# Performance work log

Measured on AMD Instinct MI355X. Metric: run time of the kernel, lower is better.

## Reference

```python
import jax, jax.numpy as jnp
import numpy as np

B, N, D = 2, 2048, 1024
H = 16
HD = D // H  # 64
NEG = -1e30


def setup_inputs() -> dict:
    key = jax.random.key(0)
    ks = jax.random.split(key, 6)
    s = 0.02
    return {
        "x": jax.random.normal(ks[0], (B, N, D), dtype=jnp.float32),
        "Wq": jax.random.normal(ks[1], (D, D), dtype=jnp.float32) * s,
        "Wk": jax.random.normal(ks[2], (D, D), dtype=jnp.float32) * s,
        "Wv": jax.random.normal(ks[3], (D, D), dtype=jnp.float32) * s,
        "Wo": jax.random.normal(ks[4], (D, D), dtype=jnp.float32) * s,
        "Wf": jax.random.normal(ks[5], (D, H), dtype=jnp.float32) * s,
    }


def reference(x, Wq, Wk, Wv, Wo, Wf):
    b, n, d = x.shape
    h, hd = H, HD
    scale = hd ** -0.5
    # projections (Linear without bias; weights stored as [in, out])
    q = (x @ Wq).reshape(b, n, h, hd).transpose(0, 2, 1, 3)  # b h n hd
    k = (x @ Wk).reshape(b, n, h, hd).transpose(0, 2, 1, 3)
    v = (x @ Wv).reshape(b, n, h, hd).transpose(0, 2, 1, 3)
    # per-head log forget gate, cumulative sum over positions
    log_f = jax.nn.log_sigmoid(x @ Wf).transpose(0, 2, 1)  # b h n
    c = jnp.cumsum(log_f, axis=-1)  # b h n
    # scores with additive decay bias: bias[i,j] = c[i] - c[j] (j <= i)
    scores = jnp.einsum('bhid,bhjd->bhij', q, k) * scale
    scores = scores + c[..., :, None] - c[..., None, :]
    causal = jnp.tril(jnp.ones((n, n), dtype=bool))
    scores = jnp.where(causal, scores, NEG)
    attn = jax.nn.softmax(scores, axis=-1)
    out = jnp.einsum('bhij,bhjd->bhid', attn, v)  # b h n hd
    out = out.transpose(0, 2, 1, 3).reshape(b, n, d)
    return out @ Wo
```

## Files before the change

### kernel.cpp

```cpp
#include <hip/hip_runtime.h>
#include <hip/hip_bf16.h>
#include <stdint.h>

#define NN 2048
#define DD 1024
#define HH 16
#define HDD 64
#define QBLK 64
#define KVBLK 64

typedef unsigned short u16;
typedef __attribute__((ext_vector_type(8))) __bf16 bf16x8_t;
typedef __attribute__((ext_vector_type(4))) float f32x4_t;

static __device__ __forceinline__ u16 f2bf(float f) {
  union { float f; uint32_t u; } v; v.f = f;
  uint32_t r = v.u + 0x7FFFu + ((v.u >> 16) & 1u);
  return (u16)(r >> 16);
}

static __device__ __forceinline__ uint32_t packbf2(float a, float b) {
  __hip_bfloat162 h2 = __float22bfloat162_rn(make_float2(a, b));
  union { __hip_bfloat162 hh; uint32_t u; } cvt; cvt.hh = h2;
  return cvt.u;
}

static __device__ __forceinline__ void async_copy16(const void* g, void* l) {
  __builtin_amdgcn_global_load_lds((const __attribute__((address_space(1))) void*)g,
                                   (__attribute__((address_space(3))) void*)l, 16, 0, 0);
}

__global__ void prep_kernel(const float* __restrict__ x, const float* __restrict__ Wf,
                            float* __restrict__ lf, u16* __restrict__ xb,
                            const float* __restrict__ W0, const float* __restrict__ W1,
                            const float* __restrict__ W2, const float* __restrict__ W3,
                            u16* __restrict__ Wt) {
  __shared__ float xs[DD];
  __shared__ float part[16][17];
  __shared__ float tile[64][65];
  int t = threadIdx.x;
  if (blockIdx.x < 4096) {
    int row = blockIdx.x;
    float4 v = *(const float4*)&x[(size_t)row * DD + t * 4];
    *(float4*)&xs[t * 4] = v;
    ushort4 o;
    o.x = f2bf(v.x); o.y = f2bf(v.y); o.z = f2bf(v.z); o.w = f2bf(v.w);
    *(ushort4*)&xb[(size_t)row * DD + t * 4] = o;
    __syncthreads();
    int h = t & 15, chunk = t >> 4;
    float s = 0.f;
#pragma unroll 8
    for (int e = 0; e < 64; e++)
      s += xs[chunk * 64 + e] * Wf[(chunk * 64 + e) * HH + h];
    part[chunk][h] = s;
    __syncthreads();
    if (t < 16) {
      float z = 0.f;
#pragma unroll
      for (int i = 0; i < 16; i++) z += part[i][t];
      float ls = fminf(z, 0.f) - log1pf(__expf(-fabsf(z)));
      int b = row >> 11, n = row & (NN - 1);
      lf[(b * HH + t) * NN + n] = ls;
    }
  } else {
    int bid = blockIdx.x - 4096;
    int wq = bid >> 8;
    const float* W = wq == 0 ? W0 : wq == 1 ? W1 : wq == 2 ? W2 : W3;
    u16* out = Wt + (size_t)wq * DD * DD;
    int bx = bid & 15;
    int by = (bid >> 4) & 15;
    int c = t & 63, r4 = t >> 6;
#pragma unroll
    for (int i = 0; i < 16; i++) {
      int row = i * 4 + r4;
      tile[row][c] = W[(by * 64 + row) * DD + bx * 64 + c];
    }
    __syncthreads();
#pragma unroll
    for (int i = 0; i < 16; i++) {
      int row = i * 4 + r4;
      out[(bx * 64 + row) * DD + by * 64 + c] = f2bf(tile[c][row]);
    }
  }
}

__global__ void cumsum_kernel(const float* __restrict__ lf, float* __restrict__ c) {
  int bh = blockIdx.x;
  int lane = threadIdx.x;
  const float* in = lf + bh * NN;
  float* out = c + bh * NN;
  float carry = 0.f;
  for (int t0 = 0; t0 < NN; t0 += 256) {
    float4 v = *(const float4*)&in[t0 + lane * 4];
    float s1 = v.x + v.y, s2 = s1 + v.z, s3 = s2 + v.w;
    float incl = s3;
#pragma unroll
    for (int off = 1; off < 64; off <<= 1) {
      float u = __shfl_up(incl, off, 64);
      if (lane >= off) incl += u;
    }
    float excl = incl - s3 + carry;
    float4 o;
    o.x = excl + v.x; o.y = excl + s1; o.z = excl + s2; o.w = excl + s3;
    *(float4*)&out[t0 + lane * 4] = o;
    carry = __shfl(incl, 63, 64) + carry;
  }
}

__global__ __launch_bounds__(512, 4) void gemm_kernel(const u16* __restrict__ A,
                                                      const u16* __restrict__ Wt,
                                                      u16* __restrict__ oQ, u16* __restrict__ oK,
                                                      u16* __restrict__ oV) {
  __shared__ u16 Als[128 * 64];
  __shared__ u16 Bls[128 * 64];
  int m0 = blockIdx.y * 128, n0 = blockIdx.x * 128;
  int tid = threadIdx.x;
  int lane = tid & 63, w = tid >> 6;
  int wm = w >> 2, wn = w & 3;
  int lr = lane & 15, lg = lane >> 4;

  const u16* gA[2]; const u16* gB[2]; u16* lA[2]; u16* lB[2];
#pragma unroll
  for (int j = 0; j < 2; j++) {
    int s = tid + j * 512;
    int row = s >> 3, ch = s & 7;
    int scol = (ch ^ (row & 7)) * 8;
    gA[j] = &A [(size_t)(m0 + row) * DD + scol];
    gB[j] = &Wt[(size_t)(n0 + row) * DD + scol];
    lA[j] = &Als[s * 8];
    lB[j] = &Bls[s * 8];
  }

  f32x4_t acc[4][2];
#pragma unroll
  for (int i = 0; i < 4; i++)
#pragma unroll
    for (int j = 0; j < 2; j++) acc[i][j] = (f32x4_t){0.f, 0.f, 0.f, 0.f};

  for (int kt = 0; kt < DD; kt += 64) {
    __syncthreads();
#pragma unroll
    for (int j = 0; j < 2; j++) {
      async_copy16(gA[j] + kt, lA[j]);
      async_copy16(gB[j] + kt, lB[j]);
    }
    __syncthreads();
#pragma unroll
    for (int kk = 0; kk < 2; kk++) {
      bf16x8_t af[4], bfv[2];
#pragma unroll
      for (int mi = 0; mi < 4; mi++) {
        int row = wm * 64 + mi * 16 + lr;
        int boff = (row * 128 + kk * 64 + lg * 16) ^ ((row & 7) << 4);
        af[mi] = *(const bf16x8_t*)((const char*)Als + boff);
      }
#pragma unroll
      for (int ni = 0; ni < 2; ni++) {
        int row = wn * 32 + ni * 16 + lr;
        int boff = (row * 128 + kk * 64 + lg * 16) ^ ((row & 7) << 4);
        bfv[ni] = *(const bf16x8_t*)((const char*)Bls + boff);
      }
#pragma unroll
      for (int mi = 0; mi < 4; mi++)
#pragma unroll
        for (int ni = 0; ni < 2; ni++)
          acc[mi][ni] = __builtin_amdgcn_mfma_f32_16x16x32_bf16(af[mi], bfv[ni], acc[mi][ni], 0, 0, 0);
    }
  }

  int which = n0 >> 10;
  int nl0 = n0 & 1023;
  if (which == 2) {
#pragma unroll
    for (int mi = 0; mi < 4; mi++)
#pragma unroll
      for (int ni = 0; ni < 2; ni++) {
        int gcol = nl0 + wn * 32 + ni * 16 + lr;
        int h = gcol >> 6, hd = gcol & 63;
        int grow0 = m0 + wm * 64 + mi * 16 + lg * 4;
        int b = grow0 >> 11, n = grow0 & (NN - 1);
        ushort4 o4;
        o4.x = f2bf(acc[mi][ni][0]);
        o4.y = f2bf(acc[mi][ni][1]);
        o4.z = f2bf(acc[mi][ni][2]);
        o4.w = f2bf(acc[mi][ni][3]);
        *(ushort4*)&oV[((size_t)(b * HH + h) * HDD + hd) * NN + n] = o4;
      }
  } else {
    u16* outp = which == 0 ? oQ : oK;
#pragma unroll
    for (int mi = 0; mi < 4; mi++)
#pragma unroll
      for (int ni = 0; ni < 2; ni++) {
        int gcol = nl0 + wn * 32 + ni * 16 + lr;
        int h = gcol >> 6, hd = gcol & 63;
#pragma unroll
        for (int r = 0; r < 4; r++) {
          int grow = m0 + wm * 64 + mi * 16 + lg * 4 + r;
          int b = grow >> 11, n = grow & (NN - 1);
          outp[((size_t)(b * HH + h) * NN + n) * HDD + hd] = f2bf(acc[mi][ni][r]);
        }
      }
  }
}

__global__ __launch_bounds__(512, 4) void gemm_out_kernel(const u16* __restrict__ A,
                                                          const u16* __restrict__ Wt,
                                                          float* __restrict__ oF) {
  __shared__ u16 Als[128 * 64];
  __shared__ u16 Bls[64 * 64];
  int m0 = blockIdx.y * 128, n0 = blockIdx.x * 64;
  int tid = threadIdx.x;
  int lane = tid & 63, w = tid >> 6;
  int wm = w >> 2, wn = w & 3;
  int lr = lane & 15, lg = lane >> 4;

  const u16* gA[2]; u16* lA[2];
#pragma unroll
  for (int j = 0; j < 2; j++) {
    int s = tid + j * 512;
    int row = s >> 3, ch = s & 7;
    int scol = (ch ^ (row & 7)) * 8;
    gA[j] = &A[(size_t)(m0 + row) * DD + scol];
    lA[j] = &Als[s * 8];
  }
  int rowb = tid >> 3, chb = tid & 7;
  const u16* gB = &Wt[(size_t)(n0 + rowb) * DD + ((chb ^ (rowb & 7)) * 8)];
  u16* lB = &Bls[tid * 8];

  f32x4_t acc[4];
#pragma unroll
  for (int i = 0; i < 4; i++) acc[i] = (f32x4_t){0.f, 0.f, 0.f, 0.f};

  for (int kt = 0; kt < DD; kt += 64) {
    __syncthreads();
#pragma unroll
    for (int j = 0; j < 2; j++) async_copy16(gA[j] + kt, lA[j]);
    async_copy16(gB + kt, lB);
    __syncthreads();
#pragma unroll
    for (int kk = 0; kk < 2; kk++) {
      bf16x8_t af[4], bf1;
#pragma unroll
      for (int mi = 0; mi < 4; mi++) {
        int row = wm * 64 + mi * 16 + lr;
        int boff = (row * 128 + kk * 64 + lg * 16) ^ ((row & 7) << 4);
        af[mi] = *(const bf16x8_t*)((const char*)Als + boff);
      }
      {
        int row = wn * 16 + lr;
        int boff = (row * 128 + kk * 64 + lg * 16) ^ ((row & 7) << 4);
        bf1 = *(const bf16x8_t*)((const char*)Bls + boff);
      }
#pragma unroll
      for (int mi = 0; mi < 4; mi++)
        acc[mi] = __builtin_amdgcn_mfma_f32_16x16x32_bf16(af[mi], bf1, acc[mi], 0, 0, 0);
    }
  }

#pragma unroll
  for (int mi = 0; mi < 4; mi++) {
    int gcol = n0 + wn * 16 + lr;
#pragma unroll
    for (int r = 0; r < 4; r++) {
      int grow = m0 + wm * 64 + mi * 16 + lg * 4 + r;
      oF[(size_t)grow * DD + gcol] = acc[mi][r];
    }
  }
}

__global__ __launch_bounds__(256) void attn_kernel(const u16* __restrict__ Q,
                                                   const u16* __restrict__ K,
                                                   const u16* __restrict__ Vt,
                                                   const float* __restrict__ cw,
                                                   u16* __restrict__ O) {
  __shared__ u16 Kls[2][KVBLK * 64];
  __shared__ u16 Vls[2][64 * KVBLK];
  int flat = blockIdx.y * gridDim.x + blockIdx.x;
  int swz = (flat & 7) * 64 + (flat >> 3);
  int pidx = swz & 15, bh = swz >> 4;
  int tid = threadIdx.x;
  int lane = tid & 63, w = tid >> 6;
  int lr = lane & 15, lg = lane >> 4;
  const u16* Qh = Q + (size_t)bh * NN * HDD;
  const u16* Kh = K + (size_t)bh * NN * HDD;
  const u16* Vh = Vt + (size_t)bh * HDD * NN;
  const float* ch = cw + bh * NN;
  int b = bh >> 4, h = bh & 15;

  int s0 = tid, s1 = tid + 256;
  int r0 = s0 >> 3, p0 = s0 & 7;
  int r1 = s1 >> 3, p1 = s1 & 7;
  const u16* gk0 = &Kh[(size_t)r0 * HDD + ((p0 ^ (r0 & 7)) * 8)];
  const u16* gk1 = &Kh[(size_t)r1 * HDD + ((p1 ^ (r1 & 7)) * 8)];
  const u16* gv0 = &Vh[(size_t)r0 * NN + ((p0 ^ (r0 & 7)) * 8)];
  const u16* gv1 = &Vh[(size_t)r1 * NN + ((p1 ^ (r1 & 7)) * 8)];

  for (int which = 0; which < 2; which++) {
    int tile = which == 0 ? (31 - pidx) : pidx;
    int qb = tile * QBLK + w * 16;
    int iq = qb + lr;

    bf16x8_t qf[2];
#pragma unroll
    for (int s = 0; s < 2; s++)
      qf[s] = *(const bf16x8_t*)&Qh[(size_t)iq * HDD + s * 32 + lg * 8];
    float cq = ch[iq];

    float lsum = 0.f;
    f32x4_t oacc[4];
#pragma unroll
    for (int fn = 0; fn < 4; fn++) oacc[fn] = (f32x4_t){0.f, 0.f, 0.f, 0.f};

    async_copy16(gk0, &Kls[0][s0 * 8]);
    async_copy16(gk1, &Kls[0][s1 * 8]);
    async_copy16(gv0, &Vls[0][s0 * 8]);
    async_copy16(gv1, &Vls[0][s1 * 8]);
    __syncthreads();

    int cur = 0;
    for (int kvt = 0; kvt <= tile; kvt++) {
      if (kvt < tile) {
        int nb = cur ^ 1;
        size_t kvn = (size_t)(kvt + 1) * KVBLK;
        async_copy16(gk0 + kvn * HDD, &Kls[nb][s0 * 8]);
        async_copy16(gk1 + kvn * HDD, &Kls[nb][s1 * 8]);
        async_copy16(gv0 + kvn, &Vls[nb][s0 * 8]);
        async_copy16(gv1 + kvn, &Vls[nb][s1 * 8]);
      }
      int kv0 = kvt * KVBLK;
      const u16* Kb = Kls[cur];
      const u16* Vb = Vls[cur];
      float4 ckv[4];
#pragma unroll
      for (int f = 0; f < 4; f++)
        ckv[f] = *(const float4*)&ch[kv0 + f * 16 + lg * 4];

      f32x4_t sacc[4];
#pragma unroll
      for (int f = 0; f < 4; f++) sacc[f] = (f32x4_t){0.f, 0.f, 0.f, 0.f};
      __builtin_amdgcn_s_setprio(1);
#pragma unroll
      for (int f = 0; f < 4; f++) {
        int row = f * 16 + lr;
#pragma unroll
        for (int s = 0; s < 2; s++) {
          int boff = (row * 128 + s * 64 + lg * 16) ^ ((row & 7) << 4);
          bf16x8_t kf = *(const bf16x8_t*)((const char*)Kb + boff);
          sacc[f] = __builtin_amdgcn_mfma_f32_16x16x32_bf16(kf, qf[s], sacc[f], 0, 0, 0);
        }
      }
      __builtin_amdgcn_s_setprio(0);

      bool diag = (kvt == tile);
      float pv[4][4];
#pragma unroll
      for (int f = 0; f < 4; f++) {
        const float* ckp = &ckv[f].x;
#pragma unroll
        for (int r = 0; r < 4; r++) {
          float val = fmaf(sacc[f][r], 0.125f, cq - ckp[r]);
          float e = __expf(val);
          if (diag && (kv0 + f * 16 + lg * 4 + r) > iq) e = 0.f;
          pv[f][r] = e; lsum += e;
        }
      }

      uint32_t wq[4][2];
#pragma unroll
      for (int f = 0; f < 4; f++) {
        wq[f][0] = packbf2(pv[f][0], pv[f][1]);
        wq[f][1] = packbf2(pv[f][2], pv[f][3]);
      }
      bf16x8_t pa[2];
#pragma unroll
      for (int s = 0; s < 2; s++) {
        uint32_t x0 = wq[2 * s][0], x1 = wq[2 * s][1];
        uint32_t y0 = wq[2 * s + 1][0], y1 = wq[2 * s + 1][1];
        asm volatile("v_permlane32_swap_b32 %0, %1" : "+v"(x0), "+v"(y0));
        asm volatile("v_permlane32_swap_b32 %0, %1" : "+v"(x1), "+v"(y1));
        asm volatile("v_permlane16_swap_b32 %0, %1" : "+v"(x0), "+v"(y0));
        asm volatile("v_permlane16_swap_b32 %0, %1" : "+v"(x1), "+v"(y1));
        union { uint32_t u[4]; bf16x8_t v; } pk;
        pk.u[0] = x0; pk.u[1] = x1; pk.u[2] = y0; pk.u[3] = y1;
        pa[s] = pk.v;
      }

      __builtin_amdgcn_s_setprio(1);
#pragma unroll
      for (int fn = 0; fn < 4; fn++) {
        int row = fn * 16 + lr;
#pragma unroll
        for (int s = 0; s < 2; s++) {
          int boff = (row * 128 + s * 64 + lg * 16) ^ ((row & 7) << 4);
          bf16x8_t vf = *(const bf16x8_t*)((const char*)Vb + boff);
          oacc[fn] = __builtin_amdgcn_mfma_f32_16x16x32_bf16(vf, pa[s], oacc[fn], 0, 0, 0);
        }
      }
      __builtin_amdgcn_s_setprio(0);
      __syncthreads();
      cur ^= 1;
    }

    lsum += __shfl_xor(lsum, 16, 64);
    lsum += __shfl_xor(lsum, 32, 64);
    float rinv = 1.0f / lsum;

    u16* orow = O + ((size_t)(b * NN + iq)) * DD + h * HDD;
#pragma unroll
    for (int fn = 0; fn < 4; fn++) {
      ushort4 o4;
      o4.x = f2bf(oacc[fn][0] * rinv);
      o4.y = f2bf(oacc[fn][1] * rinv);
      o4.z = f2bf(oacc[fn][2] * rinv);
      o4.w = f2bf(oacc[fn][3] * rinv);
      *(ushort4*)&orow[fn * 16 + lg * 4] = o4;
    }
  }
}

extern "C" void kernel_launch(void* const* d_in, const int* in_sizes, int n_in,
                              void* d_out, int out_size, void* d_ws, size_t ws_size,
                              hipStream_t stream) {
  const float* x  = (const float*)d_in[0];
  const float* Wq = (const float*)d_in[1];
  const float* Wk = (const float*)d_in[2];
  const float* Wv = (const float*)d_in[3];
  const float* Wo = (const float*)d_in[4];
  const float* Wf = (const float*)d_in[5];
  float* out = (float*)d_out;
  char* ws = (char*)d_ws;
  const size_t MB = 1024 * 1024;
  u16* x_bf  = (u16*)(ws + 0);
  u16* WqkvT = (u16*)(ws + 8 * MB);
  u16* Qw    = (u16*)(ws + 16 * MB);
  u16* Kw    = (u16*)(ws + 24 * MB);
  u16* Vw    = (u16*)(ws + 32 * MB);
  u16* Ow    = (u16*)(ws + 40 * MB);
  float* lf  = (float*)(ws + 48 * MB);
  float* cwp = (float*)(ws + 48 * MB + 262144);

  prep_kernel<<<5120, 256, 0, stream>>>(x, Wf, lf, x_bf, Wq, Wk, Wv, Wo, WqkvT);
  cumsum_kernel<<<32, 64, 0, stream>>>(lf, cwp);
  gemm_kernel<<<dim3(24, 32), 512, 0, stream>>>(x_bf, WqkvT, Qw, Kw, Vw);
  attn_kernel<<<dim3(16, 32), 256, 0, stream>>>(Qw, Kw, Vw, cwp, Ow);
  gemm_out_kernel<<<dim3(16, 32), 512, 0, stream>>>(Ow, WqkvT + (size_t)3 * DD * DD, out);
}
```

Before: 120.4 us.

## Split attention KV range across two blocks and merge partials in combine kernel

```diff
diff --git a/kernel.cpp b/kernel.cpp
--- a/kernel.cpp
+++ b/kernel.cpp
@@ -13,16 +13,29 @@
 typedef __attribute__((ext_vector_type(8))) __bf16 bf16x8_t;
 typedef __attribute__((ext_vector_type(4))) float f32x4_t;
 
+#define LOG2E 1.44269504f
+
 static __device__ __forceinline__ u16 f2bf(float f) {
   union { float f; uint32_t u; } v; v.f = f;
   uint32_t r = v.u + 0x7FFFu + ((v.u >> 16) & 1u);
   return (u16)(r >> 16);
 }
 
+static __device__ __forceinline__ float bf2f(u16 h) {
+  union { uint32_t u; float f; } v; v.u = ((uint32_t)h) << 16;
+  return v.f;
+}
+
 static __device__ __forceinline__ uint32_t packbf2(float a, float b) {
   __hip_bfloat162 h2 = __float22bfloat162_rn(make_float2(a, b));
   union { __hip_bfloat162 hh; uint32_t u; } cvt; cvt.hh = h2;
   return cvt.u;
+}
+
+static __device__ __forceinline__ float exp2_raw(float x) {
+  float r;
+  asm("v_exp_f32 %0, %1" : "=v"(r) : "v"(x));
+  return r;
 }
 
 static __device__ __forceinline__ void async_copy16(const void* g, void* l) {
@@ -101,7 +114,8 @@
     }
     float excl = incl - s3 + carry;
     float4 o;
-    o.x = excl + v.x; o.y = excl + s1; o.z = excl + s2; o.w = excl + s3;
+    o.x = (excl + v.x) * LOG2E; o.y = (excl + s1) * LOG2E;
+    o.z = (excl + s2) * LOG2E; o.w = (excl + s3) * LOG2E;
     *(float4*)&out[t0 + lane * 4] = o;
     carry = __shfl(incl, 63, 64) + carry;
   }
@@ -273,12 +287,15 @@
                                                    const u16* __restrict__ K,
                                                    const u16* __restrict__ Vt,
                                                    const float* __restrict__ cw,
-                                                   u16* __restrict__ O) {
+                                                   u16* __restrict__ PO0, u16* __restrict__ PO1,
+                                                   float* __restrict__ PL0, float* __restrict__ PL1) {
   __shared__ u16 Kls[2][KVBLK * 64];
   __shared__ u16 Vls[2][64 * KVBLK];
-  int flat = blockIdx.y * gridDim.x + blockIdx.x;
-  int swz = (flat & 7) * 64 + (flat >> 3);
-  int pidx = swz & 15, bh = swz >> 4;
+  int flat = blockIdx.x;
+  int swz = (flat & 7) * 128 + (flat >> 3);
+  int bh = swz >> 5;
+  int pidx = (swz >> 1) & 15;
+  int split = swz & 1;
   int tid = threadIdx.x;
   int lane = tid & 63, w = tid >> 6;
   int lr = lane & 15, lg = lane >> 4;
@@ -286,7 +303,10 @@
   const u16* Kh = K + (size_t)bh * NN * HDD;
   const u16* Vh = Vt + (size_t)bh * HDD * NN;
   const float* ch = cw + bh * NN;
-  int b = bh >> 4, h = bh & 15;
+  u16* po = split ? PO1 : PO0;
+  float* pl = split ? PL1 : PL0;
+
+  const float SCL = 0.125f * LOG2E;
 
   int s0 = tid, s1 = tid + 256;
   int r0 = s0 >> 3, p0 = s0 & 7;
@@ -301,6 +321,11 @@
     int qb = tile * QBLK + w * 16;
     int iq = qb + lr;
 
+    int nt = tile + 1;
+    int half = nt >> 1;
+    int kstart = split ? half : 0;
+    int kend   = split ? nt : half;
+
     bf16x8_t qf[2];
 #pragma unroll
     for (int s = 0; s < 2; s++)
@@ -312,111 +337,132 @@
 #pragma unroll
     for (int fn = 0; fn < 4; fn++) oacc[fn] = (f32x4_t){0.f, 0.f, 0.f, 0.f};
 
-    async_copy16(gk0, &Kls[0][s0 * 8]);
-    async_copy16(gk1, &Kls[0][s1 * 8]);
-    async_copy16(gv0, &Vls[0][s0 * 8]);
-    async_copy16(gv1, &Vls[0][s1 * 8]);
-    __syncthreads();
-
-    int cur = 0;
-    for (int kvt = 0; kvt <= tile; kvt++) {
-      if (kvt < tile) {
-        int nb = cur ^ 1;
-        size_t kvn = (size_t)(kvt + 1) * KVBLK;
-        async_copy16(gk0 + kvn * HDD, &Kls[nb][s0 * 8]);
-        async_copy16(gk1 + kvn * HDD, &Kls[nb][s1 * 8]);
-        async_copy16(gv0 + kvn, &Vls[nb][s0 * 8]);
-        async_copy16(gv1 + kvn, &Vls[nb][s1 * 8]);
-      }
-      int kv0 = kvt * KVBLK;
-      const u16* Kb = Kls[cur];
-      const u16* Vb = Vls[cur];
-      float4 ckv[4];
-#pragma unroll
-      for (int f = 0; f < 4; f++)
-        ckv[f] = *(const float4*)&ch[kv0 + f * 16 + lg * 4];
-
-      f32x4_t sacc[4];
-#pragma unroll
-      for (int f = 0; f < 4; f++) sacc[f] = (f32x4_t){0.f, 0.f, 0.f, 0.f};
-      __builtin_amdgcn_s_setprio(1);
-#pragma unroll
-      for (int f = 0; f < 4; f++) {
-        int row = f * 16 + lr;
+    if (kstart < kend) {
+      size_t kvs = (size_t)kstart * KVBLK;
+      async_copy16(gk0 + kvs * HDD, &Kls[0][s0 * 8]);
+      async_copy16(gk1 + kvs * HDD, &Kls[0][s1 * 8]);
+      async_copy16(gv0 + kvs, &Vls[0][s0 * 8]);
+      async_copy16(gv1 + kvs, &Vls[0][s1 * 8]);
+      __syncthreads();
+
+      int cur = 0;
+      for (int kvt = kstart; kvt < kend; kvt++) {
+        if (kvt + 1 < kend) {
+          int nb = cur ^ 1;
+          size_t kvn = (size_t)(kvt + 1) * KVBLK;
+          async_copy16(gk0 + kvn * HDD, &Kls[nb][s0 * 8]);
+          async_copy16(gk1 + kvn * HDD, &Kls[nb][s1 * 8]);
+          async_copy16(gv0 + kvn, &Vls[nb][s0 * 8]);
+          async_copy16(gv1 + kvn, &Vls[nb][s1 * 8]);
+        }
+        int kv0 = kvt * KVBLK;
+        const u16* Kb = Kls[cur];
+        const u16* Vb = Vls[cur];
+        float4 ckv[4];
+#pragma unroll
+        for (int f = 0; f < 4; f++)
+          ckv[f] = *(const float4*)&ch[kv0 + f * 16 + lg * 4];
+
+        f32x4_t sacc[4];
+#pragma unroll
+        for (int f = 0; f < 4; f++) sacc[f] = (f32x4_t){0.f, 0.f, 0.f, 0.f};
+        __builtin_amdgcn_s_setprio(1);
+#pragma unroll
+        for (int f = 0; f < 4; f++) {
+          int row = f * 16 + lr;
+#pragma unroll
+          for (int s = 0; s < 2; s++) {
+            int boff = (row * 128 + s * 64 + lg * 16) ^ ((row & 7) << 4);
+            bf16x8_t kf = *(const bf16x8_t*)((const char*)Kb + boff);
+            sacc[f] = __builtin_amdgcn_mfma_f32_16x16x32_bf16(kf, qf[s], sacc[f], 0, 0, 0);
+          }
+        }
+        __builtin_amdgcn_s_setprio(0);
+
+        bool diag = (kvt == nt - 1);
+        float pv[4][4];
+#pragma unroll
+        for (int f = 0; f < 4; f++) {
+          const float* ckp = &ckv[f].x;
+#pragma unroll
+          for (int r = 0; r < 4; r++) {
+            float val = fmaf(sacc[f][r], SCL, cq - ckp[r]);
+            float e = exp2_raw(val);
+            if (diag && (kv0 + f * 16 + lg * 4 + r) > iq) e = 0.f;
+            pv[f][r] = e; lsum += e;
+          }
+        }
+
+        bf16x8_t pa[2];
 #pragma unroll
         for (int s = 0; s < 2; s++) {
-          int boff = (row * 128 + s * 64 + lg * 16) ^ ((row & 7) << 4);
-          bf16x8_t kf = *(const bf16x8_t*)((const char*)Kb + boff);
-          sacc[f] = __builtin_amdgcn_mfma_f32_16x16x32_bf16(kf, qf[s], sacc[f], 0, 0, 0);
-        }
-      }
-      __builtin_amdgcn_s_setprio(0);
-
-      bool diag = (kvt == tile);
-      float pv[4][4];
-#pragma unroll
-      for (int f = 0; f < 4; f++) {
-        const float* ckp = &ckv[f].x;
-#pragma unroll
-        for (int r = 0; r < 4; r++) {
-          float val = fmaf(sacc[f][r], 0.125f, cq - ckp[r]);
-          float e = __expf(val);
-          if (diag && (kv0 + f * 16 + lg * 4 + r) > iq) e = 0.f;
-          pv[f][r] = e; lsum += e;
-        }
-      }
-
-      uint32_t wq[4][2];
-#pragma unroll
-      for (int f = 0; f < 4; f++) {
-        wq[f][0] = packbf2(pv[f][0], pv[f][1]);
-        wq[f][1] = packbf2(pv[f][2], pv[f][3]);
-      }
-      bf16x8_t pa[2];
-#pragma unroll
-      for (int s = 0; s < 2; s++) {
-        uint32_t x0 = wq[2 * s][0], x1 = wq[2 * s][1];
-        uint32_t y0 = wq[2 * s + 1][0], y1 = wq[2 * s + 1][1];
-        asm volatile("v_permlane32_swap_b32 %0, %1" : "+v"(x0), "+v"(y0));
-        asm volatile("v_permlane32_swap_b32 %0, %1" : "+v"(x1), "+v"(y1));
-        asm volatile("v_permlane16_swap_b32 %0, %1" : "+v"(x0), "+v"(y0));
-        asm volatile("v_permlane16_swap_b32 %0, %1" : "+v"(x1), "+v"(y1));
-        union { uint32_t u[4]; bf16x8_t v; } pk;
-        pk.u[0] = x0; pk.u[1] = x1; pk.u[2] = y0; pk.u[3] = y1;
-        pa[s] = pk.v;
-      }
-
-      __builtin_amdgcn_s_setprio(1);
-#pragma unroll
-      for (int fn = 0; fn < 4; fn++) {
-        int row = fn * 16 + lr;
-#pragma unroll
-        for (int s = 0; s < 2; s++) {
-          int boff = (row * 128 + s * 64 + lg * 16) ^ ((row & 7) << 4);
-          bf16x8_t vf = *(const bf16x8_t*)((const char*)Vb + boff);
-          oacc[fn] = __builtin_amdgcn_mfma_f32_16x16x32_bf16(vf, pa[s], oacc[fn], 0, 0, 0);
-        }
-      }
-      __builtin_amdgcn_s_setprio(0);
-      __syncthreads();
-      cur ^= 1;
+          uint32_t x0 = packbf2(pv[2 * s][0], pv[2 * s][1]);
+          uint32_t x1 = packbf2(pv[2 * s][2], pv[2 * s][3]);
+          uint32_t y0 = packbf2(pv[2 * s + 1][0], pv[2 * s + 1][1]);
+          uint32_t y1 = packbf2(pv[2 * s + 1][2], pv[2 * s + 1][3]);
+          asm volatile("v_permlane32_swap_b32 %0, %1" : "+v"(x0), "+v"(y0));
+          asm volatile("v_permlane32_swap_b32 %0, %1" : "+v"(x1), "+v"(y1));
+          asm volatile("v_permlane16_swap_b32 %0, %1" : "+v"(x0), "+v"(y0));
+          asm volatile("v_permlane16_swap_b32 %0, %1" : "+v"(x1), "+v"(y1));
+          union { uint32_t u[4]; bf16x8_t v; } pk;
+          pk.u[0] = x0; pk.u[1] = x1; pk.u[2] = y0; pk.u[3] = y1;
+          pa[s] = pk.v;
+        }
+
+        __builtin_amdgcn_s_setprio(1);
+#pragma unroll
+        for (int fn = 0; fn < 4; fn++) {
+          int row = fn * 16 + lr;
+#pragma unroll
+          for (int s = 0; s < 2; s++) {
+            int boff = (row * 128 + s * 64 + lg * 16) ^ ((row & 7) << 4);
+            bf16x8_t vf = *(const bf16x8_t*)((const char*)Vb + boff);
+            oacc[fn] = __builtin_amdgcn_mfma_f32_16x16x32_bf16(vf, pa[s], oacc[fn], 0, 0, 0);
+          }
+        }
+        __builtin_amdgcn_s_setprio(0);
+        __syncthreads();
+        cur ^= 1;
+      }
     }
 
     lsum += __shfl_xor(lsum, 16, 64);
     lsum += __shfl_xor(lsum, 32, 64);
-    float rinv = 1.0f / lsum;
-
-    u16* orow = O + ((size_t)(b * NN + iq)) * DD + h * HDD;
+
+    size_t rowbase = ((size_t)bh * NN + iq) * HDD;
 #pragma unroll
     for (int fn = 0; fn < 4; fn++) {
       ushort4 o4;
-      o4.x = f2bf(oacc[fn][0] * rinv);
-      o4.y = f2bf(oacc[fn][1] * rinv);
-      o4.z = f2bf(oacc[fn][2] * rinv);
-      o4.w = f2bf(oacc[fn][3] * rinv);
-      *(ushort4*)&orow[fn * 16 + lg * 4] = o4;
-    }
-  }
+      o4.x = f2bf(oacc[fn][0]);
+      o4.y = f2bf(oacc[fn][1]);
+      o4.z = f2bf(oacc[fn][2]);
+      o4.w = f2bf(oacc[fn][3]);
+      *(ushort4*)&po[rowbase + fn * 16 + lg * 4] = o4;
+    }
+    if (lg == 0) pl[(size_t)bh * NN + iq] = lsum;
+  }
+}
+
+__global__ void combine_kernel(const u16* __restrict__ PO0, const u16* __restrict__ PO1,
+                               const float* __restrict__ PL0, const float* __restrict__ PL1,
+                               u16* __restrict__ O) {
+  int gi = blockIdx.x * 256 + threadIdx.x;
+  int rowid = gi >> 3, seg = gi & 7;
+  uint4 a = *(const uint4*)&PO0[(size_t)rowid * HDD + seg * 8];
+  uint4 bq = *(const uint4*)&PO1[(size_t)rowid * HDD + seg * 8];
+  float rinv = 1.0f / (PL0[rowid] + PL1[rowid]);
+  const uint32_t* aw = &a.x; const uint32_t* bw = &bq.x;
+  union { u16 v[8]; uint4 q; } out;
+#pragma unroll
+  for (int i = 0; i < 4; i++) {
+    float f0 = (bf2f((u16)aw[i]) + bf2f((u16)bw[i])) * rinv;
+    float f1 = (bf2f((u16)(aw[i] >> 16)) + bf2f((u16)(bw[i] >> 16))) * rinv;
+    out.v[2 * i] = f2bf(f0);
+    out.v[2 * i + 1] = f2bf(f1);
+  }
+  int bh = rowid >> 11, n = rowid & (NN - 1);
+  int b = bh >> 4, h = bh & 15;
+  *(uint4*)&O[((size_t)(b * NN + n)) * DD + h * HDD + seg * 8] = out.q;
 }
 
 extern "C" void kernel_launch(void* const* d_in, const int* in_sizes, int n_in,
@@ -439,10 +485,15 @@
   u16* Ow    = (u16*)(ws + 40 * MB);
   float* lf  = (float*)(ws + 48 * MB);
   float* cwp = (float*)(ws + 48 * MB + 262144);
+  float* PL1 = (float*)(ws + 48 * MB + 524288);
+  u16* PO1   = (u16*)(ws + 49 * MB);
+  u16* PO0   = x_bf;
+  float* PL0 = (float*)(ws + 8 * MB);
 
   prep_kernel<<<5120, 256, 0, stream>>>(x, Wf, lf, x_bf, Wq, Wk, Wv, Wo, WqkvT);
   cumsum_kernel<<<32, 64, 0, stream>>>(lf, cwp);
   gemm_kernel<<<dim3(24, 32), 512, 0, stream>>>(x_bf, WqkvT, Qw, Kw, Vw);
-  attn_kernel<<<dim3(16, 32), 256, 0, stream>>>(Qw, Kw, Vw, cwp, Ow);
+  attn_kernel<<<1024, 256, 0, stream>>>(Qw, Kw, Vw, cwp, PO0, PO1, PL0, PL1);
+  combine_kernel<<<2048, 256, 0, stream>>>(PO0, PO1, PL0, PL1, Ow);
   gemm_out_kernel<<<dim3(16, 32), 512, 0, stream>>>(Ow, WqkvT + (size_t)3 * DD * DD, out);
 }
```

Measured after the change: 124.3 us. +3.3%, slower.
